# Optimization experiments

Hardware: AMD Instinct MI355X
Metric: run time of the kernel (lower is better)

## Reference

```python
import jax, jax.numpy as jnp
import numpy as np

B, S, E = 256, 512, 768          # batch, seq_len, embed_dim (= 2*hidden_dim)
MD = 2 * 384 + 1                 # memory feature dim after location column = 769
HOPS, OUT = 3, 3


def setup_inputs() -> dict:
    key = jax.random.key(0)
    ks = jax.random.split(key, 9)
    memory = jax.random.normal(ks[0], (B, S, E), dtype=jnp.float32)
    aspect = jax.random.normal(ks[1], (B, E), dtype=jnp.float32)
    att_w = jax.random.normal(ks[2], (MD + 2 * E,), dtype=jnp.float32) * 0.02
    att_b = jnp.zeros((1,), dtype=jnp.float32)
    gru_w_ih = jax.random.normal(ks[3], (3 * E, MD), dtype=jnp.float32) * 0.02
    gru_w_hh = jax.random.normal(ks[4], (3 * E, E), dtype=jnp.float32) * 0.02
    gru_b_ih = jnp.zeros((3 * E,), dtype=jnp.float32)
    gru_b_hh = jnp.zeros((3 * E,), dtype=jnp.float32)
    dense_w = jax.random.normal(ks[5], (E, OUT), dtype=jnp.float32) * 0.02
    dense_b = jnp.zeros((OUT,), dtype=jnp.float32)
    memory_len = jax.random.randint(ks[6], (B,), S // 2, S + 1, dtype=jnp.int32)
    left_len = jax.random.randint(ks[7], (B,), 0, 64, dtype=jnp.int32)
    aspect_len = jax.random.randint(ks[8], (B,), 1, 8, dtype=jnp.int32)
    return dict(memory=memory, aspect=aspect, att_w=att_w, att_b=att_b,
                gru_w_ih=gru_w_ih, gru_w_hh=gru_w_hh, gru_b_ih=gru_b_ih,
                gru_b_hh=gru_b_hh, dense_w=dense_w, dense_b=dense_b,
                memory_len=memory_len, left_len=left_len, aspect_len=aspect_len,
                hops=HOPS)


def _locationed_memory(memory, memory_len, left_len, aspect_len):
    # Vectorized form of the nested python loop: per-position location-decay
    # weight and signed-offset column u, only for idx < memory_len.
    dt = memory.dtype
    idx = jnp.arange(memory.shape[1], dtype=jnp.int32)[None, :]   # [1,S]
    start = left_len[:, None]
    alen = aspect_len[:, None]
    mlen = memory_len[:, None]
    before = idx < start
    after_off = idx - start - alen + 1
    u = jnp.where(before, idx - start,
                  jnp.where(idx < start + alen, 0, after_off)).astype(dt)
    l = jnp.where(before, start - idx,
                  jnp.where(idx < start + alen, 0, after_off)).astype(dt)
    valid = idx < mlen
    w = jnp.where(valid, 1.0 - l / mlen.astype(dt), 1.0)
    u = jnp.where(valid, u, 0.0)
    mem = memory * w[:, :, None]
    return jnp.concatenate([mem, u[:, :, None]], axis=-1)        # [B,S,MD]


def _gru_cell(x, h, w_ih, w_hh, b_ih, b_hh):
    gi = x @ w_ih.T + b_ih
    gh = h @ w_hh.T + b_hh
    ir, iz, in_ = jnp.split(gi, 3, axis=-1)
    hr, hz, hn = jnp.split(gh, 3, axis=-1)
    r = jax.nn.sigmoid(ir + hr)
    z = jax.nn.sigmoid(iz + hz)
    n = jnp.tanh(in_ + r * hn)
    return (1.0 - z) * n + z * h


def reference(memory, aspect, att_w, att_b, gru_w_ih, gru_w_hh, gru_b_ih,
              gru_b_hh, dense_w, dense_b, memory_len, left_len, aspect_len,
              hops):
    mem = _locationed_memory(memory, memory_len, left_len, aspect_len)
    # att_linear(cat([mem, et, aspect])) split into three small matvecs
    w_mem = att_w[:MD]
    w_et = att_w[MD:MD + E]
    w_asp = att_w[MD + E:]
    g_static = mem @ w_mem + (aspect @ w_asp)[:, None] + att_b[0]  # [B,S]
    et = jnp.zeros_like(aspect)
    for _ in range(hops):
        g = g_static + (et @ w_et)[:, None]                        # [B,S]
        alpha = jax.nn.softmax(g, axis=1)
        i = jnp.einsum('bs,bsd->bd', alpha, mem)                   # [B,MD]
        et = _gru_cell(i, et, gru_w_ih, gru_w_hh, gru_b_ih, gru_b_hh)
    logits = et @ dense_w + dense_b                                # [B,OUT]
    return logits
```

## Files before the change

### kernel.cpp

```cpp
#include <hip/hip_runtime.h>
#include <math.h>

#define Bn 256
#define Sn 512
#define En 768
#define G3n 2304

typedef __attribute__((ext_vector_type(8))) short short8;
typedef __attribute__((ext_vector_type(4))) float f32x4;

__device__ __forceinline__ float sigmoidf_(float x) { return 1.f / (1.f + __expf(-x)); }
__device__ __forceinline__ float tanhf_(float x) {
  float e = __expf(2.f * x);
  return (e - 1.f) / (e + 1.f);
}

__device__ __forceinline__ unsigned short f2bf(float x) {
  unsigned int u = __builtin_bit_cast(unsigned int, x);
  u += 0x7FFFu + ((u >> 16) & 1u);
  return (unsigned short)(u >> 16);
}
__device__ __forceinline__ float bf2f(unsigned short u) {
  unsigned int x = ((unsigned int)u) << 16;
  return __builtin_bit_cast(float, x);
}

__device__ __forceinline__ void loc_uw(int s, int start, int al, int ml, float& u, float& w) {
  float uu;
  if (s < start)            uu = (float)(s - start);
  else if (s < start + al)  uu = 0.f;
  else                      uu = (float)(s - start - al + 1);
  float l = fabsf(uu);
  if (s < ml) { w = 1.f - l / (float)ml; u = uu; }
  else        { w = 1.f; u = 0.f; }
}

__global__ __launch_bounds__(1024) void k_mega(
    const float* __restrict__ mem, const float* __restrict__ att_w,
    const int* __restrict__ mlen, const int* __restrict__ llen, const int* __restrict__ alen,
    const float* __restrict__ w_ih, const float* __restrict__ w_hh,
    float* __restrict__ pacc, float* __restrict__ pm,
    float* __restrict__ pz, float* __restrict__ piu,
    unsigned short* __restrict__ wi_bf, unsigned short* __restrict__ wh_bf,
    const float* __restrict__ db, float* __restrict__ out) {
  __shared__ float accL[16][En];
  __shared__ float mL[16], zL[16], iuL[16];
  int bc = blockIdx.x;
  int tid = threadIdx.x;

  if (bc >= 512) {
    int cb = bc - 512;
    int mat = cb >= 216;
    int t = (cb - mat * 216) * 1024 + tid;
    int idx = t * 8;
    int r = idx / En, c = idx - r * En;
    const float* src;
    unsigned short* dst;
    if (mat == 0) { src = w_ih + (size_t)r * 769 + c; dst = wi_bf + idx; }
    else          { src = w_hh + (size_t)r * En  + c; dst = wh_bf + idx; }
    unsigned int p[4];
#pragma unroll
    for (int j = 0; j < 4; ++j) {
      unsigned int lo = f2bf(src[2 * j]);
      unsigned int hi = f2bf(src[2 * j + 1]);
      p[j] = lo | (hi << 16);
    }
    *reinterpret_cast<uint4*>(dst) = make_uint4(p[0], p[1], p[2], p[3]);
    if (bc == 512 && tid < 768) out[tid] = db[tid % 3];
    return;
  }

  int b = bc >> 1, half = bc & 1;
  int wv = tid >> 6, lane = tid & 63;

  float4 w0 = *reinterpret_cast<const float4*>(att_w + lane * 4);
  float4 w1 = *reinterpret_cast<const float4*>(att_w + 256 + lane * 4);
  float4 w2 = *reinterpret_cast<const float4*>(att_w + 512 + lane * 4);
  float wtail = att_w[En];
  int start = llen[b], al = alen[b], ml = mlen[b];
  int s0row = half * 256 + wv * 16;
  const float* base = mem + ((size_t)b * Sn + s0row) * En;

  float m = -1e30f, z = 0.f, iu = 0.f;
  float4 a0 = {0, 0, 0, 0}, a1 = {0, 0, 0, 0}, a2 = {0, 0, 0, 0};
  float4 v0 = *reinterpret_cast<const float4*>(base + lane * 4);
  float4 v1 = *reinterpret_cast<const float4*>(base + 256 + lane * 4);
  float4 v2 = *reinterpret_cast<const float4*>(base + 512 + lane * 4);

  for (int r = 0; r < 16; ++r) {
    float4 c0 = v0, c1 = v1, c2 = v2;
    if (r < 15) {
      const float* nrow = base + (size_t)(r + 1) * En;
      v0 = *reinterpret_cast<const float4*>(nrow + lane * 4);
      v1 = *reinterpret_cast<const float4*>(nrow + 256 + lane * 4);
      v2 = *reinterpret_cast<const float4*>(nrow + 512 + lane * 4);
    }
    float dot = c0.x * w0.x + c0.y * w0.y + c0.z * w0.z + c0.w * w0.w
              + c1.x * w1.x + c1.y * w1.y + c1.z * w1.z + c1.w * w1.w
              + c2.x * w2.x + c2.y * w2.y + c2.z * w2.z + c2.w * w2.w;
#pragma unroll
    for (int off = 32; off; off >>= 1) dot += __shfl_xor(dot, off);
    int s = s0row + r;
    float u, w;
    loc_uw(s, start, al, ml, u, w);
    float g = w * dot + u * wtail;
    if (g > m) {
      float f = __expf(m - g);
      z *= f; iu *= f;
      a0.x *= f; a0.y *= f; a0.z *= f; a0.w *= f;
      a1.x *= f; a1.y *= f; a1.z *= f; a1.w *= f;
      a2.x *= f; a2.y *= f; a2.z *= f; a2.w *= f;
      m = g;
    }
    float e = __expf(g - m);
    z += e; iu += e * u;
    float sc = e * w;
    a0.x += sc * c0.x; a0.y += sc * c0.y; a0.z += sc * c0.z; a0.w += sc * c0.w;
    a1.x += sc * c1.x; a1.y += sc * c1.y; a1.z += sc * c1.z; a1.w += sc * c1.w;
    a2.x += sc * c2.x; a2.y += sc * c2.y; a2.z += sc * c2.z; a2.w += sc * c2.w;
  }

  *reinterpret_cast<float4*>(&accL[wv][lane * 4])       = a0;
  *reinterpret_cast<float4*>(&accL[wv][256 + lane * 4]) = a1;
  *reinterpret_cast<float4*>(&accL[wv][512 + lane * 4]) = a2;
  if (lane == 0) { mL[wv] = m; zL[wv] = z; iuL[wv] = iu; }
  __syncthreads();

  float M = mL[0];
#pragma unroll
  for (int i = 1; i < 16; ++i) M = fmaxf(M, mL[i]);
  float f[16], Z = 0.f, IU = 0.f;
#pragma unroll
  for (int i = 0; i < 16; ++i) {
    f[i] = __expf(mL[i] - M);
    Z += zL[i] * f[i];
    IU += iuL[i] * f[i];
  }
  if (tid < En) {
    float s = 0.f;
#pragma unroll
    for (int i = 0; i < 16; ++i) s += f[i] * accL[i][tid];
    pacc[(size_t)bc * En + tid] = s;
  }
  if (tid == 0) { pm[bc] = M; pz[bc] = Z; piu[bc] = IU; }
}

template <int MODE>
__global__ __launch_bounds__(512) void k_fused(
    const float* __restrict__ pacc, const float* __restrict__ pm,
    const float* __restrict__ pz, const float* __restrict__ piu,
    const unsigned short* __restrict__ Abf, const unsigned short* __restrict__ Wbf,
    const float* __restrict__ w_ih, const float* __restrict__ b_ih,
    const float* __restrict__ b_hh, float* __restrict__ gi,
    unsigned short* __restrict__ et_out_bf,
    const float* __restrict__ dw, float* __restrict__ out) {
  __shared__ __align__(16) unsigned char lds[16896 + 50688];
  auto As = reinterpret_cast<unsigned short(*)[264]>(lds);
  auto Bs = reinterpret_cast<unsigned short(*)[32][264]>(lds + 16896);
  float* red = reinterpret_cast<float*>(lds + 16896);
  __shared__ float rowF0[32], rowF1[32], rowAu[32];

  int e0 = blockIdx.x * 32, m0 = blockIdx.y * 32;
  int tid = threadIdx.x;
  int lane = tid & 63, wv = tid >> 6;
  int p = wv & 3, kh = wv >> 2;
  int wm = p >> 1, we = p & 1;
  int l15 = lane & 15, l4 = lane >> 4;

  if (MODE == 0 && tid < 32) {
    int m = m0 + tid;
    float ma = pm[2 * m], mb = pm[2 * m + 1];
    float M = fmaxf(ma, mb);
    float f0 = __expf(ma - M), f1 = __expf(mb - M);
    float iv = 1.f / (pz[2 * m] * f0 + pz[2 * m + 1] * f1);
    rowF0[tid] = f0 * iv;
    rowF1[tid] = f1 * iv;
    rowAu[tid] = (piu[2 * m] * f0 + piu[2 * m + 1] * f1) * iv;
  }

  f32x4 acc[3];
#pragma unroll
  for (int g = 0; g < 3; ++g) { acc[g][0] = 0.f; acc[g][1] = 0.f; acc[g][2] = 0.f; acc[g][3] = 0.f; }

  for (int kb = 0; kb < 3; ++kb) {
    int kbase = kb * 256;
    __syncthreads();
    if (MODE == 0) {
#pragma unroll
      for (int i = 0; i < 2; ++i) {
        int idx = tid + i * 512;
        int row = idx >> 5, ch = idx & 31;
        float f0 = rowF0[row], f1 = rowF1[row];
        const float* q0 = pacc + (size_t)(2 * (m0 + row)) * En + kbase + ch * 8;
        const float* q1 = q0 + En;
        float4 x0 = *reinterpret_cast<const float4*>(q0);
        float4 x1 = *reinterpret_cast<const float4*>(q0 + 4);
        float4 y0 = *reinterpret_cast<const float4*>(q1);
        float4 y1 = *reinterpret_cast<const float4*>(q1 + 4);
        unsigned int pk[4];
        pk[0] = (unsigned int)f2bf(f0 * x0.x + f1 * y0.x)
              | ((unsigned int)f2bf(f0 * x0.y + f1 * y0.y) << 16);
        pk[1] = (unsigned int)f2bf(f0 * x0.z + f1 * y0.z)
              | ((unsigned int)f2bf(f0 * x0.w + f1 * y0.w) << 16);
        pk[2] = (unsigned int)f2bf(f0 * x1.x + f1 * y1.x)
              | ((unsigned int)f2bf(f0 * x1.y + f1 * y1.y) << 16);
        pk[3] = (unsigned int)f2bf(f0 * x1.z + f1 * y1.z)
              | ((unsigned int)f2bf(f0 * x1.w + f1 * y1.w) << 16);
        *reinterpret_cast<uint4*>(&As[row][ch * 8]) = make_uint4(pk[0], pk[1], pk[2], pk[3]);
      }
    } else {
#pragma unroll
      for (int i = 0; i < 2; ++i) {
        int idx = tid + i * 512;
        int row = idx >> 5, ch = idx & 31;
        *reinterpret_cast<uint4*>(&As[row][ch * 8]) =
            *reinterpret_cast<const uint4*>(Abf + (size_t)(m0 + row) * En + kbase + ch * 8);
      }
    }
#pragma unroll
    for (int i = 0; i < 6; ++i) {
      int idx = tid + i * 512;
      int g = idx >> 10, rem = idx & 1023;
      int row = rem >> 5, ch = rem & 31;
      *reinterpret_cast<uint4*>(&Bs[g][row][ch * 8]) =
          *reinterpret_cast<const uint4*>(Wbf + (size_t)(g * En + e0 + row) * En + kbase + ch * 8);
    }
    __syncthreads();
#pragma unroll
    for (int ks = 0; ks < 4; ++ks) {
      int col = kh * 128 + ks * 32 + l4 * 8;
      short8 a = *reinterpret_cast<const short8*>(&As[wm * 16 + l15][col]);
#pragma unroll
      for (int g = 0; g < 3; ++g) {
        short8 bfr = *reinterpret_cast<const short8*>(&Bs[g][we * 16 + l15][col]);
        acc[g] = __builtin_amdgcn_mfma_f32_16x16x32_bf16(a, bfr, acc[g], 0, 0, 0);
      }
    }
  }

  __syncthreads();
  if (kh == 1) {
#pragma unroll
    for (int g = 0; g < 3; ++g)
#pragma unroll
      for (int j = 0; j < 4; ++j) red[(p * 64 + lane) * 17 + g * 4 + j] = acc[g][j];
  }
  __syncthreads();
  if (kh == 1) return;
#pragma unroll
  for (int g = 0; g < 3; ++g)
#pragma unroll
    for (int j = 0; j < 4; ++j) acc[g][j] += red[(p * 64 + lane) * 17 + g * 4 + j];

  int ecol = e0 + we * 16 + l15;
  int mbase = m0 + wm * 16 + l4 * 4;
  float bhr = b_hh[ecol], bhz = b_hh[En + ecol], bhn = b_hh[2 * En + ecol];
  float vout[4];
  if (MODE == 0) {
    float wn0 = w_ih[(size_t)ecol * 769 + En];
    float wn1 = w_ih[(size_t)(En + ecol) * 769 + En];
    float wn2 = w_ih[(size_t)(2 * En + ecol) * 769 + En];
    float bi0 = b_ih[ecol], bi1 = b_ih[En + ecol], bi2 = b_ih[2 * En + ecol];
#pragma unroll
    for (int j = 0; j < 4; ++j) {
      int m = mbase + j;
      float au = rowAu[wm * 16 + l4 * 4 + j];
      float gr = acc[0][j] + au * wn0 + bi0;
      float gz = acc[1][j] + au * wn1 + bi1;
      float gn = acc[2][j] + au * wn2 + bi2;
      gi[(size_t)m * G3n + ecol]          = gr;
      gi[(size_t)m * G3n + En + ecol]     = gz;
      gi[(size_t)m * G3n + 2 * En + ecol] = gn;
      float r = sigmoidf_(gr + bhr);
      float z = sigmoidf_(gz + bhz);
      float n = tanhf_(gn + r * bhn);
      vout[j] = (1.f - z) * n;
    }
  } else {
#pragma unroll
    for (int j = 0; j < 4; ++j) {
      int m = mbase + j;
      float rr = sigmoidf_(gi[(size_t)m * G3n + ecol] + acc[0][j] + bhr);
      float zz = sigmoidf_(gi[(size_t)m * G3n + En + ecol] + acc[1][j] + bhz);
      float nn = tanhf_(gi[(size_t)m * G3n + 2 * En + ecol] + rr * (acc[2][j] + bhn));
      float h = bf2f(Abf[(size_t)m * En + ecol]);
      vout[j] = (1.f - zz) * nn + zz * h;
    }
  }

  if (MODE != 2) {
#pragma unroll
    for (int j = 0; j < 4; ++j)
      et_out_bf[(size_t)(mbase + j) * En + ecol] = f2bf(vout[j]);
  } else {
    float dw0 = dw[ecol * 3 + 0], dw1 = dw[ecol * 3 + 1], dw2 = dw[ecol * 3 + 2];
    float pp[4][3];
#pragma unroll
    for (int j = 0; j < 4; ++j) {
      pp[j][0] = vout[j] * dw0;
      pp[j][1] = vout[j] * dw1;
      pp[j][2] = vout[j] * dw2;
    }
#pragma unroll
    for (int off = 1; off < 16; off <<= 1)
#pragma unroll
      for (int j = 0; j < 4; ++j) {
        pp[j][0] += __shfl_xor(pp[j][0], off);
        pp[j][1] += __shfl_xor(pp[j][1], off);
        pp[j][2] += __shfl_xor(pp[j][2], off);
      }
    if (l15 == 0) {
#pragma unroll
      for (int j = 0; j < 4; ++j) {
        atomicAdd(&out[(mbase + j) * 3 + 0], pp[j][0]);
        atomicAdd(&out[(mbase + j) * 3 + 1], pp[j][1]);
        atomicAdd(&out[(mbase + j) * 3 + 2], pp[j][2]);
      }
    }
  }
}

extern "C" void kernel_launch(void* const* d_in, const int* in_sizes, int n_in,
                              void* d_out, int out_size, void* d_ws, size_t ws_size,
                              hipStream_t stream) {
  const float* memory   = (const float*)d_in[0];
  const float* att_w    = (const float*)d_in[2];
  const float* gru_w_ih = (const float*)d_in[4];
  const float* gru_w_hh = (const float*)d_in[5];
  const float* gru_b_ih = (const float*)d_in[6];
  const float* gru_b_hh = (const float*)d_in[7];
  const float* dense_w  = (const float*)d_in[8];
  const float* dense_b  = (const float*)d_in[9];
  const int* memory_len = (const int*)d_in[10];
  const int* left_len   = (const int*)d_in[11];
  const int* aspect_len = (const int*)d_in[12];
  float* out = (float*)d_out;

  unsigned short* wi_bf  = (unsigned short*)d_ws;
  unsigned short* wh_bf  = wi_bf + (size_t)G3n * En;
  unsigned short* eta_bf = wh_bf + (size_t)G3n * En;
  unsigned short* etb_bf = eta_bf + (size_t)Bn * En;
  float* pm     = (float*)(etb_bf + (size_t)Bn * En);
  float* pz     = pm + 2 * Bn;
  float* piu    = pz + 2 * Bn;
  float* pacc   = piu + 2 * Bn;
  float* gi     = pacc + (size_t)2 * Bn * En;

  k_mega<<<dim3(944), 1024, 0, stream>>>(memory, att_w, memory_len, left_len, aspect_len,
                                         gru_w_ih, gru_w_hh, pacc, pm, pz, piu, wi_bf, wh_bf,
                                         dense_b, out);
  k_fused<0><<<dim3(En / 32, Bn / 32), 512, 0, stream>>>(
      pacc, pm, pz, piu, nullptr, wi_bf, gru_w_ih, gru_b_ih, gru_b_hh, gi, eta_bf,
      nullptr, nullptr);
  k_fused<1><<<dim3(En / 32, Bn / 32), 512, 0, stream>>>(
      nullptr, nullptr, nullptr, nullptr, eta_bf, wh_bf, nullptr, nullptr, gru_b_hh, gi, etb_bf,
      nullptr, nullptr);
  k_fused<2><<<dim3(En / 32, Bn / 32), 512, 0, stream>>>(
      nullptr, nullptr, nullptr, nullptr, etb_bf, wh_bf, nullptr, nullptr, gru_b_hh, gi, nullptr,
      dense_w, out);
}
```

Before: 116.6 us.

## Halve GRU GEMM k-tile and store gate inputs in per-thread fragment layout

The fused GRU kernel's k-loop now uses 128-wide tiles over six iterations instead of 256-wide over three. This roughly halves LDS use per block and should allow more resident blocks. The saved input-gate values (with the r/z hidden biases folded in) are now stored in a per-block, per-thread contiguous layout written and read as vector f32x4 accesses, replacing scattered strided scalar accesses across the 2304-wide gi rows. The cost is more syncthreads per block, and the gi buffer now depends on the grid shape matching between modes.

```diff
diff --git a/kernel.cpp b/kernel.cpp
--- a/kernel.cpp
+++ b/kernel.cpp
@@ -154,13 +154,14 @@
     const float* __restrict__ b_hh, float* __restrict__ gi,
     unsigned short* __restrict__ et_out_bf,
     const float* __restrict__ dw, float* __restrict__ out) {
-  __shared__ __align__(16) unsigned char lds[16896 + 50688];
-  auto As = reinterpret_cast<unsigned short(*)[264]>(lds);
-  auto Bs = reinterpret_cast<unsigned short(*)[32][264]>(lds + 16896);
-  float* red = reinterpret_cast<float*>(lds + 16896);
+  __shared__ __align__(16) unsigned char lds[8704 + 26112];
+  auto As = reinterpret_cast<unsigned short(*)[136]>(lds);
+  auto Bs = reinterpret_cast<unsigned short(*)[32][136]>(lds + 8704);
+  float* red = reinterpret_cast<float*>(lds + 8704);
   __shared__ float rowF0[32], rowF1[32], rowAu[32];
 
   int e0 = blockIdx.x * 32, m0 = blockIdx.y * 32;
+  int blockflat = blockIdx.y * 24 + blockIdx.x;
   int tid = threadIdx.x;
   int lane = tid & 63, wv = tid >> 6;
   int p = wv & 3, kh = wv >> 2;
@@ -182,53 +183,44 @@
 #pragma unroll
   for (int g = 0; g < 3; ++g) { acc[g][0] = 0.f; acc[g][1] = 0.f; acc[g][2] = 0.f; acc[g][3] = 0.f; }
 
-  for (int kb = 0; kb < 3; ++kb) {
-    int kbase = kb * 256;
+  int arow = tid >> 4, ach = tid & 15;
+  for (int kb = 0; kb < 6; ++kb) {
+    int kbase = kb * 128;
     __syncthreads();
     if (MODE == 0) {
-#pragma unroll
-      for (int i = 0; i < 2; ++i) {
-        int idx = tid + i * 512;
-        int row = idx >> 5, ch = idx & 31;
-        float f0 = rowF0[row], f1 = rowF1[row];
-        const float* q0 = pacc + (size_t)(2 * (m0 + row)) * En + kbase + ch * 8;
-        const float* q1 = q0 + En;
-        float4 x0 = *reinterpret_cast<const float4*>(q0);
-        float4 x1 = *reinterpret_cast<const float4*>(q0 + 4);
-        float4 y0 = *reinterpret_cast<const float4*>(q1);
-        float4 y1 = *reinterpret_cast<const float4*>(q1 + 4);
-        unsigned int pk[4];
-        pk[0] = (unsigned int)f2bf(f0 * x0.x + f1 * y0.x)
-              | ((unsigned int)f2bf(f0 * x0.y + f1 * y0.y) << 16);
-        pk[1] = (unsigned int)f2bf(f0 * x0.z + f1 * y0.z)
-              | ((unsigned int)f2bf(f0 * x0.w + f1 * y0.w) << 16);
-        pk[2] = (unsigned int)f2bf(f0 * x1.x + f1 * y1.x)
-              | ((unsigned int)f2bf(f0 * x1.y + f1 * y1.y) << 16);
-        pk[3] = (unsigned int)f2bf(f0 * x1.z + f1 * y1.z)
-              | ((unsigned int)f2bf(f0 * x1.w + f1 * y1.w) << 16);
-        *reinterpret_cast<uint4*>(&As[row][ch * 8]) = make_uint4(pk[0], pk[1], pk[2], pk[3]);
-      }
+      float f0 = rowF0[arow], f1 = rowF1[arow];
+      const float* q0 = pacc + (size_t)(2 * (m0 + arow)) * En + kbase + ach * 8;
+      const float* q1 = q0 + En;
+      float4 x0 = *reinterpret_cast<const float4*>(q0);
+      float4 x1 = *reinterpret_cast<const float4*>(q0 + 4);
+      float4 y0 = *reinterpret_cast<const float4*>(q1);
+      float4 y1 = *reinterpret_cast<const float4*>(q1 + 4);
+      unsigned int pk[4];
+      pk[0] = (unsigned int)f2bf(f0 * x0.x + f1 * y0.x)
+            | ((unsigned int)f2bf(f0 * x0.y + f1 * y0.y) << 16);
+      pk[1] = (unsigned int)f2bf(f0 * x0.z + f1 * y0.z)
+            | ((unsigned int)f2bf(f0 * x0.w + f1 * y0.w) << 16);
+      pk[2] = (unsigned int)f2bf(f0 * x1.x + f1 * y1.x)
+            | ((unsigned int)f2bf(f0 * x1.y + f1 * y1.y) << 16);
+      pk[3] = (unsigned int)f2bf(f0 * x1.z + f1 * y1.z)
+            | ((unsigned int)f2bf(f0 * x1.w + f1 * y1.w) << 16);
+      *reinterpret_cast<uint4*>(&As[arow][ach * 8]) = make_uint4(pk[0], pk[1], pk[2], pk[3]);
     } else {
-#pragma unroll
-      for (int i = 0; i < 2; ++i) {
-        int idx = tid + i * 512;
-        int row = idx >> 5, ch = idx & 31;
-        *reinterpret_cast<uint4*>(&As[row][ch * 8]) =
-            *reinterpret_cast<const uint4*>(Abf + (size_t)(m0 + row) * En + kbase + ch * 8);
-      }
-    }
-#pragma unroll
-    for (int i = 0; i < 6; ++i) {
+      *reinterpret_cast<uint4*>(&As[arow][ach * 8]) =
+          *reinterpret_cast<const uint4*>(Abf + (size_t)(m0 + arow) * En + kbase + ach * 8);
+    }
+#pragma unroll
+    for (int i = 0; i < 3; ++i) {
       int idx = tid + i * 512;
-      int g = idx >> 10, rem = idx & 1023;
-      int row = rem >> 5, ch = rem & 31;
+      int g = idx >> 9, rem = idx & 511;
+      int row = rem >> 4, ch = rem & 15;
       *reinterpret_cast<uint4*>(&Bs[g][row][ch * 8]) =
           *reinterpret_cast<const uint4*>(Wbf + (size_t)(g * En + e0 + row) * En + kbase + ch * 8);
     }
     __syncthreads();
 #pragma unroll
-    for (int ks = 0; ks < 4; ++ks) {
-      int col = kh * 128 + ks * 32 + l4 * 8;
+    for (int ks = 0; ks < 2; ++ks) {
+      int col = kh * 64 + ks * 32 + l4 * 8;
       short8 a = *reinterpret_cast<const short8*>(&As[wm * 16 + l15][col]);
 #pragma unroll
       for (int g = 0; g < 3; ++g) {
@@ -254,35 +246,41 @@
 
   int ecol = e0 + we * 16 + l15;
   int mbase = m0 + wm * 16 + l4 * 4;
-  float bhr = b_hh[ecol], bhz = b_hh[En + ecol], bhn = b_hh[2 * En + ecol];
+  float* gfrag = gi + ((size_t)blockflat * 256 + tid) * 12;
   float vout[4];
   if (MODE == 0) {
+    float bhr = b_hh[ecol], bhz = b_hh[En + ecol], bhn = b_hh[2 * En + ecol];
     float wn0 = w_ih[(size_t)ecol * 769 + En];
     float wn1 = w_ih[(size_t)(En + ecol) * 769 + En];
     float wn2 = w_ih[(size_t)(2 * En + ecol) * 769 + En];
     float bi0 = b_ih[ecol], bi1 = b_ih[En + ecol], bi2 = b_ih[2 * En + ecol];
+    f32x4 R, Z, N;
 #pragma unroll
     for (int j = 0; j < 4; ++j) {
       int m = mbase + j;
       float au = rowAu[wm * 16 + l4 * 4 + j];
-      float gr = acc[0][j] + au * wn0 + bi0;
-      float gz = acc[1][j] + au * wn1 + bi1;
-      float gn = acc[2][j] + au * wn2 + bi2;
-      gi[(size_t)m * G3n + ecol]          = gr;
-      gi[(size_t)m * G3n + En + ecol]     = gz;
-      gi[(size_t)m * G3n + 2 * En + ecol] = gn;
-      float r = sigmoidf_(gr + bhr);
-      float z = sigmoidf_(gz + bhz);
-      float n = tanhf_(gn + r * bhn);
+      R[j] = acc[0][j] + au * wn0 + bi0 + bhr;
+      Z[j] = acc[1][j] + au * wn1 + bi1 + bhz;
+      N[j] = acc[2][j] + au * wn2 + bi2;
+      float r = sigmoidf_(R[j]);
+      float z = sigmoidf_(Z[j]);
+      float n = tanhf_(N[j] + r * bhn);
       vout[j] = (1.f - z) * n;
     }
+    *reinterpret_cast<f32x4*>(gfrag)     = R;
+    *reinterpret_cast<f32x4*>(gfrag + 4) = Z;
+    *reinterpret_cast<f32x4*>(gfrag + 8) = N;
   } else {
+    float bhn = b_hh[2 * En + ecol];
+    f32x4 R = *reinterpret_cast<const f32x4*>(gfrag);
+    f32x4 Z = *reinterpret_cast<const f32x4*>(gfrag + 4);
+    f32x4 N = *reinterpret_cast<const f32x4*>(gfrag + 8);
 #pragma unroll
     for (int j = 0; j < 4; ++j) {
       int m = mbase + j;
-      float rr = sigmoidf_(gi[(size_t)m * G3n + ecol] + acc[0][j] + bhr);
-      float zz = sigmoidf_(gi[(size_t)m * G3n + En + ecol] + acc[1][j] + bhz);
-      float nn = tanhf_(gi[(size_t)m * G3n + 2 * En + ecol] + rr * (acc[2][j] + bhn));
+      float rr = sigmoidf_(R[j] + acc[0][j]);
+      float zz = sigmoidf_(Z[j] + acc[1][j]);
+      float nn = tanhf_(N[j] + rr * (acc[2][j] + bhn));
       float h = bf2f(Abf[(size_t)m * En + ecol]);
       vout[j] = (1.f - zz) * nn + zz * h;
     }
```

New measurement: 120.6 us. +3.4%, slower.
